# Optimization experiments

Measured on AMD Instinct MI355X. Metric: run time of the kernel, lower is better.

## Reference

```python
import jax, jax.numpy as jnp
import numpy as np

N_NODES = 20000
N_EDGES = 320000
IN_CH = 64
GROWTH = 64
N_BLOCKS = 3


def setup_inputs() -> dict:
    key = jax.random.key(0)
    ks = jax.random.split(key, 8)
    x = jax.random.normal(ks[0], (N_NODES, IN_CH), dtype=jnp.float32)
    edge_index = jax.random.randint(ks[1], (2, N_EDGES), 0, N_NODES, dtype=jnp.int32)
    params = {}
    for i in range(N_BLOCKS):
        fan_in = 2 * (IN_CH + i * GROWTH)
        scale = 1.0 / np.sqrt(fan_in)
        params[f"W{i}"] = jax.random.normal(ks[2 + i], (fan_in, GROWTH), dtype=jnp.float32) * scale
        params[f"b{i}"] = jnp.zeros((GROWTH,), dtype=jnp.float32)
    return {"x": x, "W0": params["W0"], "b0": params["b0"],
            "W1": params["W1"], "b1": params["b1"],
            "W2": params["W2"], "b2": params["b2"],
            "edge_index": edge_index}


def _edge_conv(x, src, dst, W, b, n_nodes):
    # PyG EdgeConv: message = nn(cat[x_i, x_j - x_i]), aggr='max'
    xi = x[dst]                                   # target features  [E, C]
    xj = x[src]                                   # source features  [E, C]
    feat = jnp.concatenate([xi, xj - xi], axis=-1)  # [E, 2C]
    msg = jax.nn.relu(feat @ W + b)               # [E, growth]
    agg = jax.ops.segment_max(msg, dst, num_segments=n_nodes)  # [N, growth]
    # nodes with no incoming edges -> identity (-inf) replaced by 0 (PyG scatter-max behavior)
    return jnp.where(jnp.isfinite(agg), agg, 0.0)


def reference(x, W0, b0, W1, b1, W2, b2, edge_index):
    src, dst = edge_index[0], edge_index[1]
    n = x.shape[0]
    for W, b in ((W0, b0), (W1, b1), (W2, b2)):
        out = _edge_conv(x, src, dst, W, b, n)
        x = jnp.concatenate([x, out], axis=-1)    # dense connectivity
    # [N, growth*(n_blocks+1)] -> [N, growth, n_blocks+1] (row-major, same as torch)
    x = x.reshape(n, GROWTH, N_BLOCKS + 1)
    return jnp.max(x, axis=-1)
```

## Files before the change

### kernel.cpp

```cpp
#include <hip/hip_runtime.h>
#include <hip/hip_bf16.h>

#define NN 20000
#define NE 320000
#define XSTB 256
#define CAP 96

typedef __attribute__((ext_vector_type(8))) short short8v;
typedef __attribute__((ext_vector_type(4))) float float4v;

struct bh4 { __hip_bfloat16 a, b, c, d; };

#define WT_OFF1 0
#define WT_OFF2 (128 * 128)
#define WT_TOT  (128 * 128 + 128 * 192)

__device__ __forceinline__ float bucket_max(const int* __restrict__ el, int c, int lane,
                                            const __hip_bfloat16* __restrict__ Pbb) {
    float mx = -INFINITY;
    int i = 0;
    for (; i + 4 <= c; i += 4) {
        int s0 = el[i], s1 = el[i + 1], s2 = el[i + 2], s3 = el[i + 3];
        float v0 = __bfloat162float(Pbb[(size_t)s0 * 64 + lane]);
        float v1 = __bfloat162float(Pbb[(size_t)s1 * 64 + lane]);
        float v2 = __bfloat162float(Pbb[(size_t)s2 * 64 + lane]);
        float v3 = __bfloat162float(Pbb[(size_t)s3 * 64 + lane]);
        mx = fmaxf(mx, fmaxf(fmaxf(v0, v1), fmaxf(v2, v3)));
    }
    for (; i < c; ++i)
        mx = fmaxf(mx, __bfloat162float(Pbb[(size_t)el[i] * 64 + lane]));
    return mx;
}

__global__ __launch_bounds__(256) void kz_kernel(int* __restrict__ cursor) {
    int q = blockIdx.x * 256 + threadIdx.x;
    if (q < NN / 4) *((int4*)cursor + q) = make_int4(0, 0, 0, 0);
}

__global__ __launch_bounds__(256, 4) void k1_kernel(
    const float* __restrict__ x, const float* __restrict__ W0,
    const float* __restrict__ W1, const float* __restrict__ W2,
    const int* __restrict__ esrc, const int* __restrict__ edst,
    __hip_bfloat16* __restrict__ xcatb, __hip_bfloat16* __restrict__ Wt,
    int* __restrict__ cursor, int* __restrict__ elist,
    float* __restrict__ Pa, __hip_bfloat16* __restrict__ Pbb) {
    __shared__ __hip_bfloat16 Ws0[128][72];
    int blk = blockIdx.x, tid = threadIdx.x;
    int w = tid >> 6, lane = tid & 63;

    if (blk < 625) {
        for (int e = tid; e < 4096; e += 256) {
            int r = e >> 6, j = e & 63;
            float wt = W0[r * 64 + j];
            float wb = W0[(64 + r) * 64 + j];
            Ws0[j][r] = __float2bfloat16(wt - wb);
            Ws0[64 + j][r] = __float2bfloat16(wb);
        }
        __syncthreads();
        int wid = blk * 4 + w;
        int panel = wid >> 1, half = wid & 1;
        int m = lane & 15, g = lane >> 4;
        const float* aptr = x + (size_t)(panel * 16 + m) * 64 + g * 8;
        float4v acc[4] = {{0.f,0.f,0.f,0.f},{0.f,0.f,0.f,0.f},
                          {0.f,0.f,0.f,0.f},{0.f,0.f,0.f,0.f}};
#pragma unroll
        for (int k0 = 0; k0 < 64; k0 += 32) {
            float4 a0 = *(const float4*)(aptr + k0);
            float4 a1 = *(const float4*)(aptr + k0 + 4);
            __hip_bfloat16 ah[8] = {
                __float2bfloat16(a0.x), __float2bfloat16(a0.y),
                __float2bfloat16(a0.z), __float2bfloat16(a0.w),
                __float2bfloat16(a1.x), __float2bfloat16(a1.y),
                __float2bfloat16(a1.z), __float2bfloat16(a1.w)};
            short8v a = *(const short8v*)ah;
#pragma unroll
            for (int t = 0; t < 4; ++t) {
                short8v bb = *(const short8v*)(&Ws0[half * 64 + t * 16 + m][k0 + g * 8]);
                acc[t] = __builtin_amdgcn_mfma_f32_16x16x32_bf16(a, bb, acc[t], 0, 0, 0);
            }
        }
        int r0 = panel * 16;
        if (half == 0) {
#pragma unroll
            for (int t = 0; t < 4; ++t)
#pragma unroll
                for (int r = 0; r < 4; ++r)
                    Pa[(size_t)(r0 + g * 4 + r) * 64 + t * 16 + m] = acc[t][r];
        } else {
#pragma unroll
            for (int t = 0; t < 4; ++t)
#pragma unroll
                for (int r = 0; r < 4; ++r)
                    Pbb[(size_t)(r0 + g * 4 + r) * 64 + t * 16 + m] =
                        __float2bfloat16(acc[t][r]);
        }
    } else if (blk < 1875) {
        int i = (blk - 625) * 256 + tid;
        int d = edst[i];
        int pos = atomicAdd(cursor + d, 1);
        if (pos < CAP) elist[(size_t)d * CAP + pos] = esrc[i];
    } else if (blk < 3125) {
        int i = (blk - 1875) * 256 + tid;
        int n = i >> 4, c4 = (i & 15) << 2;
        float4 v = *(const float4*)(x + (size_t)n * 64 + c4);
        bh4 o = {__float2bfloat16(v.x), __float2bfloat16(v.y),
                 __float2bfloat16(v.z), __float2bfloat16(v.w)};
        *(bh4*)(xcatb + (size_t)n * XSTB + c4) = o;
    } else {
        int e = (blk - 3125) * 256 + tid;
        const float* W;
        int K, off;
        if (e < WT_OFF2) { W = W1; K = 128; off = WT_OFF1; }
        else             { W = W2; K = 192; off = WT_OFF2; }
        int el = e - off;
        int j = el / K, k = el - j * K;
        float wv;
        if (j < 64) wv = W[(size_t)k * 64 + j] - W[(size_t)(K + k) * 64 + j];
        else        wv = W[(size_t)(K + k) * 64 + (j - 64)];
        Wt[(size_t)off + (size_t)j * K + k] = __float2bfloat16(wv);
    }
}

template <int C>
__global__ __launch_bounds__(256, 4) void fused_kernel(
    const float* __restrict__ PaIn, const __hip_bfloat16* __restrict__ PbbIn,
    const float* __restrict__ b, const int* __restrict__ cnt,
    const int* __restrict__ elist, __hip_bfloat16* __restrict__ xcatb,
    const __hip_bfloat16* __restrict__ Wt, float* __restrict__ PaOut,
    __hip_bfloat16* __restrict__ PbbOut) {
    __shared__ __hip_bfloat16 newt[16][72];
    int tid = threadIdx.x;
    int w = tid >> 6, lane = tid & 63;
    int panel = blockIdx.x;
    int r0 = panel * 16;

#pragma unroll
    for (int nl = 0; nl < 4; ++nl) {
        int local = w * 4 + nl;
        int node = r0 + local;
        int c = cnt[node];
        if (c > CAP) c = CAP;
        float mx = bucket_max(elist + (size_t)node * CAP, c, lane, PbbIn);
        float v = fmaxf(PaIn[(size_t)node * 64 + lane] + b[lane] + mx, 0.f);
        __hip_bfloat16 h = __float2bfloat16(v);
        newt[local][lane] = h;
        xcatb[(size_t)node * XSTB + (C - 64) + lane] = h;
    }
    __syncthreads();
    if (w >= 2) return;

    int half = w;
    int m = lane & 15, g = lane >> 4;
    const __hip_bfloat16* aptr = xcatb + (size_t)(r0 + m) * XSTB + g * 8;
    const __hip_bfloat16* bptr = Wt + (size_t)(half * 64 + m) * C + g * 8;
    float4v acc[4] = {{0.f,0.f,0.f,0.f},{0.f,0.f,0.f,0.f},
                      {0.f,0.f,0.f,0.f},{0.f,0.f,0.f,0.f}};
#pragma unroll
    for (int k0 = 0; k0 < C; k0 += 32) {
        short8v a;
        if (k0 < C - 64) a = *(const short8v*)(aptr + k0);
        else             a = *(const short8v*)(&newt[m][k0 - (C - 64) + g * 8]);
#pragma unroll
        for (int t = 0; t < 4; ++t) {
            short8v bb = *(const short8v*)(bptr + (size_t)t * 16 * C + k0);
            acc[t] = __builtin_amdgcn_mfma_f32_16x16x32_bf16(a, bb, acc[t], 0, 0, 0);
        }
    }
    if (half == 0) {
#pragma unroll
        for (int t = 0; t < 4; ++t)
#pragma unroll
            for (int r = 0; r < 4; ++r)
                PaOut[(size_t)(r0 + g * 4 + r) * 64 + t * 16 + m] = acc[t][r];
    } else {
#pragma unroll
        for (int t = 0; t < 4; ++t)
#pragma unroll
            for (int r = 0; r < 4; ++r)
                PbbOut[(size_t)(r0 + g * 4 + r) * 64 + t * 16 + m] =
                    __float2bfloat16(acc[t][r]);
    }
}

__global__ __launch_bounds__(256, 4) void aggf_kernel(
    const float* __restrict__ Pa, const __hip_bfloat16* __restrict__ Pbb,
    const float* __restrict__ b, const int* __restrict__ cnt,
    const int* __restrict__ elist, const __hip_bfloat16* __restrict__ xcatb,
    float* __restrict__ out) {
    __shared__ float sm[4][64];
    int w = threadIdx.x >> 6, lane = threadIdx.x & 63;
    int node = blockIdx.x * 4 + w;
    int c = cnt[node];
    if (c > CAP) c = CAP;
    float mx = bucket_max(elist + (size_t)node * CAP, c, lane, Pbb);
    float v = fmaxf(Pa[(size_t)node * 64 + lane] + b[lane] + mx, 0.f);
    sm[w][lane] = v;
    float m;
    if (lane < 48) {
        bh4 q = *(const bh4*)(xcatb + (size_t)node * XSTB + (lane << 2));
        float f0 = __bfloat162float(q.a), f1 = __bfloat162float(q.b);
        float f2 = __bfloat162float(q.c), f3 = __bfloat162float(q.d);
        m = fmaxf(fmaxf(f0, f1), fmaxf(f2, f3));
    } else {
        const float* p = &sm[w][(lane - 48) << 2];
        m = fmaxf(fmaxf(p[0], p[1]), fmaxf(p[2], p[3]));
    }
    out[(size_t)node * 64 + lane] = m;
}

extern "C" void kernel_launch(void* const* d_in, const int* in_sizes, int n_in,
                              void* d_out, int out_size, void* d_ws, size_t ws_size,
                              hipStream_t stream) {
    const float* x = (const float*)d_in[0];
    const float* W0 = (const float*)d_in[1];
    const float* W1 = (const float*)d_in[3];
    const float* W2 = (const float*)d_in[5];
    const float* b0 = (const float*)d_in[2];
    const float* b1 = (const float*)d_in[4];
    const float* b2 = (const float*)d_in[6];
    const int* eidx = (const int*)d_in[7];
    const int* esrc = eidx;
    const int* edst = eidx + NE;
    float* out = (float*)d_out;

    char* w = (char*)d_ws;
    __hip_bfloat16* xcatb = (__hip_bfloat16*)w;  w += (size_t)NN * XSTB * 2;
    float* PaA = (float*)w;                      w += (size_t)NN * 64 * 4;
    __hip_bfloat16* PbbA = (__hip_bfloat16*)w;   w += (size_t)NN * 64 * 2;
    float* PaB = (float*)w;                      w += (size_t)NN * 64 * 4;
    __hip_bfloat16* PbbB = (__hip_bfloat16*)w;   w += (size_t)NN * 64 * 2;
    __hip_bfloat16* Wt = (__hip_bfloat16*)w;     w += (size_t)WT_TOT * 2;
    int* cursor = (int*)w;                       w += (size_t)NN * 4;
    int* elist = (int*)w;

    kz_kernel<<<20, 256, 0, stream>>>(cursor);
    k1_kernel<<<3285, 256, 0, stream>>>(x, W0, W1, W2, esrc, edst, xcatb, Wt,
                                        cursor, elist, PaA, PbbA);
    fused_kernel<128><<<1250, 256, 0, stream>>>(PaA, PbbA, b0, cursor, elist, xcatb,
                                                Wt + WT_OFF1, PaB, PbbB);
    fused_kernel<192><<<1250, 256, 0, stream>>>(PaB, PbbB, b1, cursor, elist, xcatb,
                                                Wt + WT_OFF2, PaA, PbbA);
    aggf_kernel<<<5000, 256, 0, stream>>>(PaA, PbbA, b2, cursor, elist, xcatb, out);
}
```

Baseline: 90.52 us.

## Vectorize edge-list gathers and precompute W0 transpose in zero-init kernel

The neighbor max-aggregation loop now loads edge indices as int4 pairs and issues 8 gathers at once. In the fused kernel all four nodes of a wave are interleaved so up to 32 loads are in flight, which is meant to hide gather latency. The W0 transpose/split moves from every GEMM block's shared-memory prologue into the zero-init kernel, so the k1 GEMM reads pre-transposed bf16 weights from global memory instead. The trade-offs are more registers, extra masked iterations when bucket counts differ, and elist reads padded past the count (which stay inside the CAP-sized slot).

New measurement: 129.5 us. 1.43x slower.

```diff
diff --git a/kernel.cpp b/kernel.cpp
--- a/kernel.cpp
+++ b/kernel.cpp
@@ -11,56 +11,51 @@
 
 struct bh4 { __hip_bfloat16 a, b, c, d; };
 
-#define WT_OFF1 0
-#define WT_OFF2 (128 * 128)
-#define WT_TOT  (128 * 128 + 128 * 192)
-
-__device__ __forceinline__ float bucket_max(const int* __restrict__ el, int c, int lane,
-                                            const __hip_bfloat16* __restrict__ Pbb) {
-    float mx = -INFINITY;
-    int i = 0;
-    for (; i + 4 <= c; i += 4) {
-        int s0 = el[i], s1 = el[i + 1], s2 = el[i + 2], s3 = el[i + 3];
-        float v0 = __bfloat162float(Pbb[(size_t)s0 * 64 + lane]);
-        float v1 = __bfloat162float(Pbb[(size_t)s1 * 64 + lane]);
-        float v2 = __bfloat162float(Pbb[(size_t)s2 * 64 + lane]);
-        float v3 = __bfloat162float(Pbb[(size_t)s3 * 64 + lane]);
-        mx = fmaxf(mx, fmaxf(fmaxf(v0, v1), fmaxf(v2, v3)));
-    }
-    for (; i < c; ++i)
-        mx = fmaxf(mx, __bfloat162float(Pbb[(size_t)el[i] * 64 + lane]));
-    return mx;
-}
-
-__global__ __launch_bounds__(256) void kz_kernel(int* __restrict__ cursor) {
-    int q = blockIdx.x * 256 + threadIdx.x;
-    if (q < NN / 4) *((int4*)cursor + q) = make_int4(0, 0, 0, 0);
+#define WT_OFF0 0
+#define WT_OFF1 (128 * 64)
+#define WT_OFF2 (WT_OFF1 + 128 * 128)
+#define WT_TOT  (WT_OFF2 + 128 * 192)
+
+__global__ __launch_bounds__(256) void kz_kernel(const float* __restrict__ W0,
+                                                 const float* __restrict__ W1,
+                                                 const float* __restrict__ W2,
+                                                 __hip_bfloat16* __restrict__ Wt,
+                                                 int* __restrict__ cursor) {
+    int blk = blockIdx.x, tid = threadIdx.x;
+    if (blk < 20) {
+        int q = blk * 256 + tid;
+        if (q < NN / 4) *((int4*)cursor + q) = make_int4(0, 0, 0, 0);
+    } else {
+        int e = (blk - 20) * 256 + tid;
+        const float* W;
+        int K, off;
+        if (e < WT_OFF1) { W = W0; K = 64;  off = WT_OFF0; }
+        else if (e < WT_OFF2) { W = W1; K = 128; off = WT_OFF1; }
+        else { W = W2; K = 192; off = WT_OFF2; }
+        int el = e - off;
+        int j = el / K, k = el - j * K;
+        float wv;
+        if (j < 64) wv = W[(size_t)k * 64 + j] - W[(size_t)(K + k) * 64 + j];
+        else        wv = W[(size_t)(K + k) * 64 + (j - 64)];
+        Wt[(size_t)off + (size_t)j * K + k] = __float2bfloat16(wv);
+    }
 }
 
 __global__ __launch_bounds__(256, 4) void k1_kernel(
-    const float* __restrict__ x, const float* __restrict__ W0,
-    const float* __restrict__ W1, const float* __restrict__ W2,
+    const float* __restrict__ x, const __hip_bfloat16* __restrict__ Wt,
     const int* __restrict__ esrc, const int* __restrict__ edst,
-    __hip_bfloat16* __restrict__ xcatb, __hip_bfloat16* __restrict__ Wt,
-    int* __restrict__ cursor, int* __restrict__ elist,
-    float* __restrict__ Pa, __hip_bfloat16* __restrict__ Pbb) {
-    __shared__ __hip_bfloat16 Ws0[128][72];
+    __hip_bfloat16* __restrict__ xcatb, int* __restrict__ cursor,
+    int* __restrict__ elist, float* __restrict__ Pa,
+    __hip_bfloat16* __restrict__ Pbb) {
     int blk = blockIdx.x, tid = threadIdx.x;
     int w = tid >> 6, lane = tid & 63;
 
     if (blk < 625) {
-        for (int e = tid; e < 4096; e += 256) {
-            int r = e >> 6, j = e & 63;
-            float wt = W0[r * 64 + j];
-            float wb = W0[(64 + r) * 64 + j];
-            Ws0[j][r] = __float2bfloat16(wt - wb);
-            Ws0[64 + j][r] = __float2bfloat16(wb);
-        }
-        __syncthreads();
         int wid = blk * 4 + w;
         int panel = wid >> 1, half = wid & 1;
         int m = lane & 15, g = lane >> 4;
         const float* aptr = x + (size_t)(panel * 16 + m) * 64 + g * 8;
+        const __hip_bfloat16* bptr = Wt + (size_t)(half * 64 + m) * 64 + g * 8;
         float4v acc[4] = {{0.f,0.f,0.f,0.f},{0.f,0.f,0.f,0.f},
                           {0.f,0.f,0.f,0.f},{0.f,0.f,0.f,0.f}};
 #pragma unroll
@@ -75,7 +70,7 @@
             short8v a = *(const short8v*)ah;
 #pragma unroll
             for (int t = 0; t < 4; ++t) {
-                short8v bb = *(const short8v*)(&Ws0[half * 64 + t * 16 + m][k0 + g * 8]);
+                short8v bb = *(const short8v*)(bptr + (size_t)t * 16 * 64 + k0);
                 acc[t] = __builtin_amdgcn_mfma_f32_16x16x32_bf16(a, bb, acc[t], 0, 0, 0);
             }
         }
@@ -99,25 +94,13 @@
         int d = edst[i];
         int pos = atomicAdd(cursor + d, 1);
         if (pos < CAP) elist[(size_t)d * CAP + pos] = esrc[i];
-    } else if (blk < 3125) {
+    } else {
         int i = (blk - 1875) * 256 + tid;
         int n = i >> 4, c4 = (i & 15) << 2;
         float4 v = *(const float4*)(x + (size_t)n * 64 + c4);
         bh4 o = {__float2bfloat16(v.x), __float2bfloat16(v.y),
                  __float2bfloat16(v.z), __float2bfloat16(v.w)};
         *(bh4*)(xcatb + (size_t)n * XSTB + c4) = o;
-    } else {
-        int e = (blk - 3125) * 256 + tid;
-        const float* W;
-        int K, off;
-        if (e < WT_OFF2) { W = W1; K = 128; off = WT_OFF1; }
-        else             { W = W2; K = 192; off = WT_OFF2; }
-        int el = e - off;
-        int j = el / K, k = el - j * K;
-        float wv;
-        if (j < 64) wv = W[(size_t)k * 64 + j] - W[(size_t)(K + k) * 64 + j];
-        else        wv = W[(size_t)(K + k) * 64 + (j - 64)];
-        Wt[(size_t)off + (size_t)j * K + k] = __float2bfloat16(wv);
     }
 }
 
@@ -134,17 +117,54 @@
     int panel = blockIdx.x;
     int r0 = panel * 16;
 
+    int node0 = r0 + w * 4;
+    int cc[4];
+    float mx[4], pa[4];
+    const int* el[4];
+#pragma unroll
+    for (int nl = 0; nl < 4; ++nl) {
+        int node = node0 + nl;
+        int c = cnt[node];
+        cc[nl] = c > CAP ? CAP : c;
+        el[nl] = elist + (size_t)node * CAP;
+        mx[nl] = -INFINITY;
+        pa[nl] = PaIn[(size_t)node * 64 + lane] + b[lane];
+    }
+    int cmax = max(max(cc[0], cc[1]), max(cc[2], cc[3]));
+    for (int i = 0; i < cmax; i += 8) {
+        int4 ea[4], eb[4];
+#pragma unroll
+        for (int nl = 0; nl < 4; ++nl) {
+            ea[nl] = *(const int4*)(el[nl] + i);
+            eb[nl] = *(const int4*)(el[nl] + i + 4);
+        }
+        float v[4][8];
+#pragma unroll
+        for (int nl = 0; nl < 4; ++nl) {
+            int c = cc[nl];
+            int idx[8] = {ea[nl].x, ea[nl].y, ea[nl].z, ea[nl].w,
+                          eb[nl].x, eb[nl].y, eb[nl].z, eb[nl].w};
+#pragma unroll
+            for (int j = 0; j < 8; ++j) {
+                v[nl][j] = -INFINITY;
+                if (i + j < c)
+                    v[nl][j] = __bfloat162float(PbbIn[(size_t)idx[j] * 64 + lane]);
+            }
+        }
+#pragma unroll
+        for (int nl = 0; nl < 4; ++nl) {
+            float m0 = fmaxf(fmaxf(v[nl][0], v[nl][1]), fmaxf(v[nl][2], v[nl][3]));
+            float m1 = fmaxf(fmaxf(v[nl][4], v[nl][5]), fmaxf(v[nl][6], v[nl][7]));
+            mx[nl] = fmaxf(mx[nl], fmaxf(m0, m1));
+        }
+    }
 #pragma unroll
     for (int nl = 0; nl < 4; ++nl) {
         int local = w * 4 + nl;
-        int node = r0 + local;
-        int c = cnt[node];
-        if (c > CAP) c = CAP;
-        float mx = bucket_max(elist + (size_t)node * CAP, c, lane, PbbIn);
-        float v = fmaxf(PaIn[(size_t)node * 64 + lane] + b[lane] + mx, 0.f);
-        __hip_bfloat16 h = __float2bfloat16(v);
+        float vv = fmaxf(pa[nl] + mx[nl], 0.f);
+        __hip_bfloat16 h = __float2bfloat16(vv);
         newt[local][lane] = h;
-        xcatb[(size_t)node * XSTB + (C - 64) + lane] = h;
+        xcatb[(size_t)(node0 + nl) * XSTB + (C - 64) + lane] = h;
     }
     __syncthreads();
     if (w >= 2) return;
@@ -192,9 +212,25 @@
     int node = blockIdx.x * 4 + w;
     int c = cnt[node];
     if (c > CAP) c = CAP;
-    float mx = bucket_max(elist + (size_t)node * CAP, c, lane, Pbb);
-    float v = fmaxf(Pa[(size_t)node * 64 + lane] + b[lane] + mx, 0.f);
-    sm[w][lane] = v;
+    const int* el = elist + (size_t)node * CAP;
+    float pa = Pa[(size_t)node * 64 + lane] + b[lane];
+    float mx = -INFINITY;
+    for (int i = 0; i < c; i += 8) {
+        int4 ea = *(const int4*)(el + i);
+        int4 eb = *(const int4*)(el + i + 4);
+        int idx[8] = {ea.x, ea.y, ea.z, ea.w, eb.x, eb.y, eb.z, eb.w};
+        float v[8];
+#pragma unroll
+        for (int j = 0; j < 8; ++j) {
+            v[j] = -INFINITY;
+            if (i + j < c) v[j] = __bfloat162float(Pbb[(size_t)idx[j] * 64 + lane]);
+        }
+        float m0 = fmaxf(fmaxf(v[0], v[1]), fmaxf(v[2], v[3]));
+        float m1 = fmaxf(fmaxf(v[4], v[5]), fmaxf(v[6], v[7]));
+        mx = fmaxf(mx, fmaxf(m0, m1));
+    }
+    float vv = fmaxf(pa + mx, 0.f);
+    sm[w][lane] = vv;
     float m;
     if (lane < 48) {
         bh4 q = *(const bh4*)(xcatb + (size_t)node * XSTB + (lane << 2));
@@ -233,9 +269,9 @@
     int* cursor = (int*)w;                       w += (size_t)NN * 4;
     int* elist = (int*)w;
 
-    kz_kernel<<<20, 256, 0, stream>>>(cursor);
-    k1_kernel<<<3285, 256, 0, stream>>>(x, W0, W1, W2, esrc, edst, xcatb, Wt,
-                                        cursor, elist, PaA, PbbA);
+    kz_kernel<<<20 + 192, 256, 0, stream>>>(W0, W1, W2, Wt, cursor);
+    k1_kernel<<<3125, 256, 0, stream>>>(x, Wt, esrc, edst, xcatb, cursor, elist,
+                                        PaA, PbbA);
     fused_kernel<128><<<1250, 256, 0, stream>>>(PaA, PbbA, b0, cursor, elist, xcatb,
                                                 Wt + WT_OFF1, PaB, PbbB);
     fused_kernel<192><<<1250, 256, 0, stream>>>(PaB, PbbB, b1, cursor, elist, xcatb,
```
